# Kernel tuning notes

Hardware: AMD Instinct MI355X
Metric: run time of the kernel (lower is better)

## Reference

```python
import jax, jax.numpy as jnp
import numpy as np

DT = 0.05            # fixed implicit step size (stand-in for adaptive PID steps)
LOG2PI = 1.8378770664093453


def _unscale_p(p, pscale):
    # amici ParameterScaling: 0=none, 1=ln, 2=log10 (mirrors unscale_p vmap+stack+get)
    return jnp.select([pscale == 0, pscale == 1], [p, jnp.exp(p)], jnp.power(10.0, p))


def setup_inputs() -> dict:
    key = jax.random.key(0)
    ks = jax.random.split(key, 7)
    B, T, S, O = 512, 64, 128, 32
    return {
        "p": jax.random.normal(ks[0], (B, S), dtype=jnp.float32) * 0.1,
        "A": jax.random.normal(ks[1], (S, S), dtype=jnp.float32),
        "C": jax.random.normal(ks[2], (O, S), dtype=jnp.float32) / np.sqrt(S),
        "d": jax.random.normal(ks[3], (O,), dtype=jnp.float32),
        "sigma_p": jax.random.normal(ks[4], (O,), dtype=jnp.float32) * 0.1,
        "my": jax.random.normal(ks[5], (B, T, O), dtype=jnp.float32),
        "pscale": jax.random.randint(ks[6], (S,), 0, 3, dtype=jnp.int32),
    }


def reference(p, A, C, d, sigma_p, my, pscale):
    B, T, O = my.shape
    S = p.shape[1]
    ps = _unscale_p(p, pscale[None, :])            # [B,S] unscaled parameters
    r = jax.nn.softplus(ps)                        # per-condition decay rates > 0
    x0 = jax.nn.sigmoid(ps)                        # x0(p,k): initial state
    As = A / jnp.sqrt(jnp.asarray(S, p.dtype))     # shared coupling matrix
    I = jnp.eye(S, dtype=p.dtype)
    # implicit Euler for xdot = (As - diag(r)) x:  K x_{t+dt} = x_t
    K = I[None] - DT * As[None] + DT * r[:, :, None] * I[None]   # [B,S,S]

    def step(x, _):
        x_next = jnp.linalg.solve(K, x[..., None])[..., 0]       # batched SxS solve
        return x_next, x_next

    _, xs = jax.lax.scan(step, x0, None, length=T)               # [T,B,S]
    xs = jnp.transpose(xs, (1, 0, 2))                            # [B,T,S]

    y = jnp.einsum("bts,os->bto", xs, C) + d                    # observables
    sigy = jnp.exp(sigma_p)                                      # sigmay (per obs)
    Jy = 0.5 * jnp.square((y - my) / sigy) + jnp.log(sigy) + 0.5 * LOG2PI
    llh = -jnp.sum(Jy)                                           # _loss: -sum(Jy)
    return llh
```

## Files before the change

kernel.cpp:

```cpp
#include <hip/hip_runtime.h>
#include <math.h>

#define BB 512
#define TT 64
#define SS 128
#define OO 32
#define DTC 0.05f

#define NEG_DT_INVSQ (-0.004419417382415922f)
#define HALF_LOG2PI 0.9189385332046727f

typedef float f4 __attribute__((ext_vector_type(4)));

#define SW(r) ((((r) >> 3) & 7) << 2)

__device__ __forceinline__ f4 ld4(const float* a) { return *reinterpret_cast<const f4*>(a); }
__device__ __forceinline__ void st4(float* a, f4 v) { *reinterpret_cast<f4*>(a) = v; }

__global__ __launch_bounds__(256, 2) void fused_kernel(
    const float* __restrict__ p, const float* __restrict__ A,
    const float* __restrict__ C, const float* __restrict__ d,
    const float* __restrict__ sigma_p, const float* __restrict__ my,
    const int* __restrict__ pscale, float* __restrict__ ws_partial)
{
    __shared__ __align__(16) float Wf[SS * SS];
    __shared__ __align__(16) float PsT[8 * 12];
    __shared__ __align__(16) float xv[SS];
    __shared__ __align__(16) float ptile[16 * 132];
    __shared__ float redsm[4];

    const int tid = threadIdx.x;
    const int b = blockIdx.x;

    if (tid < SS) {
        float pv = p[b * SS + tid];
        int sc = pscale[tid];
        float ps = (sc == 0) ? pv : ((sc == 1) ? expf(pv) : exp10f(pv));
        ptile[tid] = fmaxf(ps, 0.0f) + log1pf(expf(-fabsf(ps)));
        xv[tid] = 1.0f / (1.0f + expf(-ps));
    }
    __syncthreads();

    #pragma unroll 8
    for (int it = 0; it < (SS * SS) / 256; ++it) {
        int m = it * 256 + tid;
        int i = m & (SS - 1);
        int j = m >> 7;
        float v = NEG_DT_INVSQ * A[m];
        if (i == j) v += fmaf(DTC, ptile[i], 1.0f);
        Wf[i * SS + (j ^ SW(i))] = v;
    }
    __syncthreads();

    const int ti = tid & 15;
    const int tj = tid >> 4;
    const int swt = (ti & 7) << 2;
    const int pcA = (8 * tj) ^ swt;
    const int pcB = (8 * tj + 4) ^ swt;

    for (int kb = 0; kb < 16; ++kb) {
        const int k0 = kb * 8;
        const int swk = (kb & 7) << 2;

        f4 cda[8], cdb[8];
        {
            const int qA = k0 ^ swt, qB = (k0 + 4) ^ swt;
            #pragma unroll
            for (int rr = 0; rr < 8; ++rr) {
                int base = (8 * ti + rr) * SS;
                cda[rr] = ld4(&Wf[base + qA]);
                cdb[rr] = ld4(&Wf[base + qB]);
            }
            if (ti == kb) {
                #pragma unroll
                for (int rr = 0; rr < 8; ++rr) {
                    if (rr < 4) cda[rr][rr] -= 1.0f;
                    else        cdb[rr][rr - 4] -= 1.0f;
                }
            }
        }

        if (tid < 64) {
            int gi = tid >> 3, gj = tid & 7;
            float q = Wf[(k0 + gi) * SS + ((k0 + gj) ^ swk)];
            #pragma unroll
            for (int kk = 0; kk < 8; ++kk) {
                float ck = __shfl(q, (gi << 3) | kk, 64);
                float pr = __shfl(q, (kk << 3) | gj, 64);
                float pv = __shfl(q, (kk << 3) | kk, 64);
                float ip = 1.0f / pv;
                float ckd = ck - ((gi == kk) ? 1.0f : 0.0f);
                float prd = pr + ((gj == kk) ? 1.0f : 0.0f);
                q = fmaf(-ckd, prd * ip, q);
            }
            PsT[gj * 12 + gi] = q;
        }
        __syncthreads();

        f4 ta[8] = {f4{0,0,0,0},f4{0,0,0,0},f4{0,0,0,0},f4{0,0,0,0},
                    f4{0,0,0,0},f4{0,0,0,0},f4{0,0,0,0},f4{0,0,0,0}};
        f4 tb[8] = {f4{0,0,0,0},f4{0,0,0,0},f4{0,0,0,0},f4{0,0,0,0},
                    f4{0,0,0,0},f4{0,0,0,0},f4{0,0,0,0},f4{0,0,0,0}};
        {
            const int rc0 = (8 * tj) ^ swk, rc1 = (8 * tj + 4) ^ swk;
            #pragma unroll
            for (int j = 0; j < 8; ++j) {
                int base = (k0 + j) * SS;
                f4 rwa = ld4(&Wf[base + rc0]);
                f4 rwb = ld4(&Wf[base + rc1]);
                if (tj == kb) {
                    if (j < 4) rwa[j] += 1.0f;
                    else       rwb[j - 4] += 1.0f;
                }
                f4 pa = ld4(&PsT[j * 12]);
                f4 pb = ld4(&PsT[j * 12 + 4]);
                #pragma unroll
                for (int i = 0; i < 4; ++i) {
                    ta[i] += pa[i] * rwa;  tb[i] += pa[i] * rwb;
                    ta[i + 4] += pb[i] * rwa;  tb[i + 4] += pb[i] * rwb;
                }
            }
        }
        __syncthreads();

        #pragma unroll
        for (int rr = 0; rr < 8; ++rr) {
            int base = (8 * ti + rr) * SS;
            f4 va = ld4(&Wf[base + pcA]);
            f4 vb = ld4(&Wf[base + pcB]);
            #pragma unroll
            for (int i = 0; i < 8; ++i) {
                float cdi = (i < 4) ? cda[rr][i] : cdb[rr][i - 4];
                va -= cdi * ta[i];
                vb -= cdi * tb[i];
            }
            st4(&Wf[base + pcA], va);
            st4(&Wf[base + pcB], vb);
        }
        __syncthreads();
    }

    f4 wta[8], wtb[8];
    #pragma unroll
    for (int rr = 0; rr < 8; ++rr) {
        int base = (8 * ti + rr) * SS;
        wta[rr] = ld4(&Wf[base + pcA]);
        wtb[rr] = ld4(&Wf[base + pcB]);
    }

    const int o = tid >> 3, cc = tid & 7;
    float Creg[16];
    #pragma unroll
    for (int i2 = 0; i2 < 16; ++i2) Creg[i2] = C[o * SS + i2 * 8 + cc];
    const float dval = d[o];
    const float sgp = sigma_p[o];
    const float isig = expf(-sgp);
    const float cterm = sgp + HALF_LOG2PI;
    float lacc = 0.0f;
    const float* __restrict__ myb = my + (size_t)b * (TT * OO);

    for (int t = 0; t < TT; ++t) {
        f4 xa = ld4(&xv[8 * ti]);
        f4 xb = ld4(&xv[8 * ti + 4]);
        f4 pa = {0, 0, 0, 0}, pb = {0, 0, 0, 0};
        #pragma unroll
        for (int rr = 0; rr < 8; ++rr) {
            float xr = (rr < 4) ? xa[rr] : xb[rr - 4];
            pa += xr * wta[rr];
            pb += xr * wtb[rr];
        }
        st4(&ptile[ti * 132 + 8 * tj], pa);
        st4(&ptile[ti * 132 + 8 * tj + 4], pb);
        __syncthreads();
        if (tid < SS) {
            float s = 0.0f;
            #pragma unroll
            for (int g = 0; g < 16; ++g) s += ptile[g * 132 + tid];
            xv[tid] = s;
        }
        __syncthreads();

        float py = 0.0f;
        #pragma unroll
        for (int i2 = 0; i2 < 16; ++i2)
            py = fmaf(Creg[i2], xv[i2 * 8 + cc], py);
        py += __shfl_xor(py, 1);
        py += __shfl_xor(py, 2);
        py += __shfl_xor(py, 4);
        if (cc == 0) {
            float e = (py + dval - myb[t * OO + o]) * isig;
            lacc += fmaf(0.5f * e, e, cterm);
        }
    }

    #pragma unroll
    for (int off = 32; off >= 1; off >>= 1) lacc += __shfl_xor(lacc, off);
    if ((tid & 63) == 0) redsm[tid >> 6] = lacc;
    __syncthreads();
    if (tid == 0)
        ws_partial[b] = redsm[0] + redsm[1] + redsm[2] + redsm[3];
}

__global__ void reduce_kernel(const float* __restrict__ ws_partial,
                              float* __restrict__ out)
{
    __shared__ double sm[8];
    int tid = threadIdx.x;
    double v = (double)ws_partial[tid];
    #pragma unroll
    for (int off = 32; off >= 1; off >>= 1) v += __shfl_xor(v, off);
    if ((tid & 63) == 0) sm[tid >> 6] = v;
    __syncthreads();
    if (tid == 0) {
        double s = 0.0;
        for (int i = 0; i < 8; ++i) s += sm[i];
        out[0] = (float)(-s);
    }
}

extern "C" void kernel_launch(void* const* d_in, const int* in_sizes, int n_in,
                              void* d_out, int out_size, void* d_ws, size_t ws_size,
                              hipStream_t stream) {
    const float* p       = (const float*)d_in[0];
    const float* A       = (const float*)d_in[1];
    const float* C       = (const float*)d_in[2];
    const float* d       = (const float*)d_in[3];
    const float* sigma_p = (const float*)d_in[4];
    const float* my      = (const float*)d_in[5];
    const int*   pscale  = (const int*)d_in[6];
    float* out = (float*)d_out;
    float* wsf = (float*)d_ws;

    fused_kernel<<<BB, 256, 0, stream>>>(p, A, C, d, sigma_p, my, pscale, wsf);
    reduce_kernel<<<1, 512, 0, stream>>>(wsf, out);
}
```

Before: 209.1 us.

## Use 512 threads per block and restructure time-step matvec with double-buffered state

Doubles the block size to 512 threads so each thread updates half as many columns in the blocked Gauss-Jordan inversion. The per-step matvec is restructured: each group of four threads owns one row of the inverse and reduces with shuffles, and the state is double-buffered so each time step needs one barrier instead of two. The observation projection is deferred by one step and overlapped with the next matvec. The A load is also vectorised. Register pressure under launch_bounds(512,4) and the extra warps at barriers are the tradeoff.

```diff
diff --git a/kernel.cpp b/kernel.cpp
--- a/kernel.cpp
+++ b/kernel.cpp
@@ -12,12 +12,12 @@
 
 typedef float f4 __attribute__((ext_vector_type(4)));
 
-#define SW(r) ((((r) >> 3) & 7) << 2)
+#define PSW(r) ((((r) >> 3) & 7) << 2)
 
 __device__ __forceinline__ f4 ld4(const float* a) { return *reinterpret_cast<const f4*>(a); }
 __device__ __forceinline__ void st4(float* a, f4 v) { *reinterpret_cast<f4*>(a) = v; }
 
-__global__ __launch_bounds__(256, 2) void fused_kernel(
+__global__ __launch_bounds__(512, 4) void fused_kernel(
     const float* __restrict__ p, const float* __restrict__ A,
     const float* __restrict__ C, const float* __restrict__ d,
     const float* __restrict__ sigma_p, const float* __restrict__ my,
@@ -25,9 +25,9 @@
 {
     __shared__ __align__(16) float Wf[SS * SS];
     __shared__ __align__(16) float PsT[8 * 12];
-    __shared__ __align__(16) float xv[SS];
-    __shared__ __align__(16) float ptile[16 * 132];
-    __shared__ float redsm[4];
+    __shared__ __align__(16) float xbuf[2][SS];
+    __shared__ __align__(16) float rbuf[SS];
+    __shared__ float redsm[8];
 
     const int tid = threadIdx.x;
     const int b = blockIdx.x;
@@ -36,27 +36,26 @@
         float pv = p[b * SS + tid];
         int sc = pscale[tid];
         float ps = (sc == 0) ? pv : ((sc == 1) ? expf(pv) : exp10f(pv));
-        ptile[tid] = fmaxf(ps, 0.0f) + log1pf(expf(-fabsf(ps)));
-        xv[tid] = 1.0f / (1.0f + expf(-ps));
-    }
-    __syncthreads();
-
-    #pragma unroll 8
-    for (int it = 0; it < (SS * SS) / 256; ++it) {
-        int m = it * 256 + tid;
-        int i = m & (SS - 1);
-        int j = m >> 7;
-        float v = NEG_DT_INVSQ * A[m];
-        if (i == j) v += fmaf(DTC, ptile[i], 1.0f);
-        Wf[i * SS + (j ^ SW(i))] = v;
+        rbuf[tid] = fmaxf(ps, 0.0f) + log1pf(expf(-fabsf(ps)));
+        xbuf[0][tid] = 1.0f / (1.0f + expf(-ps));
+    }
+    __syncthreads();
+
+    #pragma unroll
+    for (int it = 0; it < (SS * SS) / (512 * 4); ++it) {
+        int m4 = it * 512 + tid;
+        int j = m4 >> 5;
+        int i0 = (m4 & 31) << 2;
+        f4 v = NEG_DT_INVSQ * ld4(&A[j * SS + i0]);
+        if (j >= i0 && j < i0 + 4) v[j - i0] += fmaf(DTC, rbuf[j], 1.0f);
+        st4(&Wf[j * SS + (i0 ^ PSW(j))], v);
     }
     __syncthreads();
 
     const int ti = tid & 15;
     const int tj = tid >> 4;
     const int swt = (ti & 7) << 2;
-    const int pcA = (8 * tj) ^ swt;
-    const int pcB = (8 * tj + 4) ^ swt;
+    const int pcA = (4 * tj) ^ swt;
 
     for (int kb = 0; kb < 16; ++kb) {
         const int k0 = kb * 8;
@@ -97,27 +96,21 @@
         }
         __syncthreads();
 
-        f4 ta[8] = {f4{0,0,0,0},f4{0,0,0,0},f4{0,0,0,0},f4{0,0,0,0},
-                    f4{0,0,0,0},f4{0,0,0,0},f4{0,0,0,0},f4{0,0,0,0}};
-        f4 tb[8] = {f4{0,0,0,0},f4{0,0,0,0},f4{0,0,0,0},f4{0,0,0,0},
-                    f4{0,0,0,0},f4{0,0,0,0},f4{0,0,0,0},f4{0,0,0,0}};
+        f4 t[8] = {f4{0,0,0,0},f4{0,0,0,0},f4{0,0,0,0},f4{0,0,0,0},
+                   f4{0,0,0,0},f4{0,0,0,0},f4{0,0,0,0},f4{0,0,0,0}};
         {
-            const int rc0 = (8 * tj) ^ swk, rc1 = (8 * tj + 4) ^ swk;
+            const int rc = (4 * tj) ^ swk;
             #pragma unroll
             for (int j = 0; j < 8; ++j) {
-                int base = (k0 + j) * SS;
-                f4 rwa = ld4(&Wf[base + rc0]);
-                f4 rwb = ld4(&Wf[base + rc1]);
-                if (tj == kb) {
-                    if (j < 4) rwa[j] += 1.0f;
-                    else       rwb[j - 4] += 1.0f;
-                }
+                f4 rw = ld4(&Wf[(k0 + j) * SS + rc]);
+                if (tj == 2 * kb) { if (j < 4) rw[j] += 1.0f; }
+                else if (tj == 2 * kb + 1) { if (j >= 4) rw[j - 4] += 1.0f; }
                 f4 pa = ld4(&PsT[j * 12]);
                 f4 pb = ld4(&PsT[j * 12 + 4]);
                 #pragma unroll
                 for (int i = 0; i < 4; ++i) {
-                    ta[i] += pa[i] * rwa;  tb[i] += pa[i] * rwb;
-                    ta[i + 4] += pb[i] * rwa;  tb[i + 4] += pb[i] * rwb;
+                    t[i]     += pa[i] * rw;
+                    t[i + 4] += pb[i] * rw;
                 }
             }
         }
@@ -127,31 +120,25 @@
         for (int rr = 0; rr < 8; ++rr) {
             int base = (8 * ti + rr) * SS;
             f4 va = ld4(&Wf[base + pcA]);
-            f4 vb = ld4(&Wf[base + pcB]);
             #pragma unroll
             for (int i = 0; i < 8; ++i) {
                 float cdi = (i < 4) ? cda[rr][i] : cdb[rr][i - 4];
-                va -= cdi * ta[i];
-                vb -= cdi * tb[i];
+                va -= cdi * t[i];
             }
             st4(&Wf[base + pcA], va);
-            st4(&Wf[base + pcB], vb);
-        }
-        __syncthreads();
-    }
-
-    f4 wta[8], wtb[8];
-    #pragma unroll
-    for (int rr = 0; rr < 8; ++rr) {
-        int base = (8 * ti + rr) * SS;
-        wta[rr] = ld4(&Wf[base + pcA]);
-        wtb[rr] = ld4(&Wf[base + pcB]);
-    }
-
-    const int o = tid >> 3, cc = tid & 7;
-    float Creg[16];
-    #pragma unroll
-    for (int i2 = 0; i2 < 16; ++i2) Creg[i2] = C[o * SS + i2 * 8 + cc];
+        }
+        __syncthreads();
+    }
+
+    const int s = tid >> 2, q = tid & 3;
+    f4 Mreg[8];
+    #pragma unroll
+    for (int c = 0; c < 8; ++c)
+        Mreg[c] = ld4(&Wf[s * SS + (((32 * q) + 4 * c) ^ PSW(s))]);
+
+    const int o = tid >> 4, sub = tid & 15;
+    const f4 Cr0 = ld4(&C[o * SS + 4 * sub]);
+    const f4 Cr1 = ld4(&C[o * SS + 64 + 4 * sub]);
     const float dval = d[o];
     const float sgp = sigma_p[o];
     const float isig = expf(-sgp);
@@ -159,36 +146,46 @@
     float lacc = 0.0f;
     const float* __restrict__ myb = my + (size_t)b * (TT * OO);
 
+    int cur = 0;
     for (int t = 0; t < TT; ++t) {
-        f4 xa = ld4(&xv[8 * ti]);
-        f4 xb = ld4(&xv[8 * ti + 4]);
-        f4 pa = {0, 0, 0, 0}, pb = {0, 0, 0, 0};
+        const float* xc = xbuf[cur];
+        f4 acc = {0, 0, 0, 0};
         #pragma unroll
-        for (int rr = 0; rr < 8; ++rr) {
-            float xr = (rr < 4) ? xa[rr] : xb[rr - 4];
-            pa += xr * wta[rr];
-            pb += xr * wtb[rr];
-        }
-        st4(&ptile[ti * 132 + 8 * tj], pa);
-        st4(&ptile[ti * 132 + 8 * tj + 4], pb);
-        __syncthreads();
-        if (tid < SS) {
-            float s = 0.0f;
-            #pragma unroll
-            for (int g = 0; g < 16; ++g) s += ptile[g * 132 + tid];
-            xv[tid] = s;
-        }
-        __syncthreads();
-
-        float py = 0.0f;
-        #pragma unroll
-        for (int i2 = 0; i2 < 16; ++i2)
-            py = fmaf(Creg[i2], xv[i2 * 8 + cc], py);
+        for (int cc = 0; cc < 8; ++cc) {
+            int c = (cc + 2 * q) & 7;
+            acc += Mreg[c] * ld4(&xc[32 * q + 4 * c]);
+        }
+        float xn = (acc[0] + acc[1]) + (acc[2] + acc[3]);
+        xn += __shfl_xor(xn, 1);
+        xn += __shfl_xor(xn, 2);
+
+        if (t > 0) {
+            f4 pv4 = Cr0 * ld4(&xc[4 * sub]) + Cr1 * ld4(&xc[64 + 4 * sub]);
+            float py = (pv4[0] + pv4[1]) + (pv4[2] + pv4[3]);
+            py += __shfl_xor(py, 1);
+            py += __shfl_xor(py, 2);
+            py += __shfl_xor(py, 4);
+            py += __shfl_xor(py, 8);
+            if (sub == 0) {
+                float e = (py + dval - myb[(t - 1) * OO + o]) * isig;
+                lacc += fmaf(0.5f * e, e, cterm);
+            }
+        }
+
+        if (q == 0) xbuf[cur ^ 1][s] = xn;
+        __syncthreads();
+        cur ^= 1;
+    }
+    {
+        const float* xc = xbuf[cur];
+        f4 pv4 = Cr0 * ld4(&xc[4 * sub]) + Cr1 * ld4(&xc[64 + 4 * sub]);
+        float py = (pv4[0] + pv4[1]) + (pv4[2] + pv4[3]);
         py += __shfl_xor(py, 1);
         py += __shfl_xor(py, 2);
         py += __shfl_xor(py, 4);
-        if (cc == 0) {
-            float e = (py + dval - myb[t * OO + o]) * isig;
+        py += __shfl_xor(py, 8);
+        if (sub == 0) {
+            float e = (py + dval - myb[63 * OO + o]) * isig;
             lacc += fmaf(0.5f * e, e, cterm);
         }
     }
@@ -197,8 +194,12 @@
     for (int off = 32; off >= 1; off >>= 1) lacc += __shfl_xor(lacc, off);
     if ((tid & 63) == 0) redsm[tid >> 6] = lacc;
     __syncthreads();
-    if (tid == 0)
-        ws_partial[b] = redsm[0] + redsm[1] + redsm[2] + redsm[3];
+    if (tid == 0) {
+        float ssum = 0.0f;
+        #pragma unroll
+        for (int i = 0; i < 8; ++i) ssum += redsm[i];
+        ws_partial[b] = ssum;
+    }
 }
 
 __global__ void reduce_kernel(const float* __restrict__ ws_partial,
@@ -231,6 +232,6 @@
     float* out = (float*)d_out;
     float* wsf = (float*)d_ws;
 
-    fused_kernel<<<BB, 256, 0, stream>>>(p, A, C, d, sigma_p, my, pscale, wsf);
+    fused_kernel<<<BB, 512, 0, stream>>>(p, A, C, d, sigma_p, my, pscale, wsf);
     reduce_kernel<<<1, 512, 0, stream>>>(wsf, out);
 }
```

Result: slower. 224.2 us (+7.2%).
